# Kernel optimization log

Hardware: AMD Instinct MI355X
Metric: run time of the kernel (lower is better)

## Reference

```python
import jax, jax.numpy as jnp
import numpy as np

NEG = -100000.0  # matches torch masked_fill constant

def setup_inputs() -> dict:
    key = jax.random.key(0)
    k1, k2, k3, k4 = jax.random.split(key, 4)
    B, T, D, H, S = 8, 2048, 1024, 8, 128
    features = jax.random.normal(k1, (B, T, D), dtype=jnp.float32)
    begins = jax.random.randint(k2, (B, S), 0, 2016, dtype=jnp.int64)
    widths = jax.random.randint(k3, (B, S), 1, 33, dtype=jnp.int64)
    ends = jnp.minimum(begins + widths, T)
    key_w = jax.random.normal(k4, (H, D), dtype=jnp.float32) / np.sqrt(D)
    key_b = jnp.zeros((H,), dtype=jnp.float32)
    return {"features": features, "begins": begins, "ends": ends,
            "key_w": key_w, "key_b": key_b}


def reference(features, begins, ends, key_w, key_b):
    # features: [B, T, D]; begins/ends: [B, S]
    B, T, D = features.shape
    H = key_w.shape[0]
    S = begins.shape[1]
    pos = jnp.arange(T)  # [T]
    # span mask [B, S, T]
    mask = (begins[..., None] <= pos) & (pos < ends[..., None])
    # key projection: [B, T, H]
    logits = jnp.einsum('btd,hd->bth', features, key_w) + key_b
    # masked softmax over T per (batch, span, head): [B, S, T, H]
    masked = jnp.where(mask[..., None], logits[:, None, :, :], NEG)
    weights = jax.nn.softmax(masked, axis=-2)
    # values = features reshaped to heads: [B, T, H, D//H]
    values = features.reshape(B, T, H, D // H)
    res = jnp.einsum('bthd,bsth->bshd', values, weights)  # [B, S, H, D//H]
    return res.reshape(B, S, D)
```

## Files before the change

kernel.cpp:

```cpp
#include <hip/hip_runtime.h>

#define B_  8
#define T_  2048
#define D_  1024
#define H_  8
#define S_  128

__global__ __launch_bounds__(1024) void logits_kernel(
    const float* __restrict__ feat,
    const float* __restrict__ kw,
    const float* __restrict__ kb,
    float* __restrict__ logits)
{
    const int wv   = threadIdx.x >> 6;
    const int lane = threadIdx.x & 63;
    const int row  = blockIdx.x * 16 + wv;

    __shared__ __align__(16) float kwl[H_ * D_];

    {
        const float4* src = (const float4*)kw;
        float4*       dst = (float4*)kwl;
        dst[threadIdx.x]        = src[threadIdx.x];
        dst[threadIdx.x + 1024] = src[threadIdx.x + 1024];
    }

    const float* fr = feat + (size_t)row * D_;
    float4 fv0 = *(const float4*)(fr +   0 + lane * 4);
    float4 fv1 = *(const float4*)(fr + 256 + lane * 4);
    float4 fv2 = *(const float4*)(fr + 512 + lane * 4);
    float4 fv3 = *(const float4*)(fr + 768 + lane * 4);

    __syncthreads();

    float acc[H_];
#pragma unroll
    for (int h = 0; h < H_; ++h) {
        const float* kh = &kwl[h * D_ + lane * 4];
        float4 k0 = *(const float4*)(kh +   0);
        float4 k1 = *(const float4*)(kh + 256);
        float4 k2 = *(const float4*)(kh + 512);
        float4 k3 = *(const float4*)(kh + 768);
        acc[h] = fv0.x * k0.x + fv0.y * k0.y + fv0.z * k0.z + fv0.w * k0.w
               + fv1.x * k1.x + fv1.y * k1.y + fv1.z * k1.z + fv1.w * k1.w
               + fv2.x * k2.x + fv2.y * k2.y + fv2.z * k2.z + fv2.w * k2.w
               + fv3.x * k3.x + fv3.y * k3.y + fv3.z * k3.z + fv3.w * k3.w;
    }

#pragma unroll
    for (int s = 0; s < 3; ++s) {
        const int m = 1 << s;
        const bool hi = (lane >> s) & 1;
#pragma unroll
        for (int j = 0; j < (4 >> s); ++j) {
            float mine  = hi ? acc[2 * j + 1] : acc[2 * j];
            float other = hi ? acc[2 * j]     : acc[2 * j + 1];
            acc[j] = mine + __shfl_xor(other, m, 64);
        }
    }
    acc[0] += __shfl_xor(acc[0],  8, 64);
    acc[0] += __shfl_xor(acc[0], 16, 64);
    acc[0] += __shfl_xor(acc[0], 32, 64);

    if (lane < H_)
        logits[(size_t)row * H_ + lane] = acc[0] + kb[lane];
}

__global__ __launch_bounds__(256) void pool_kernel(
    const float* __restrict__ feat,
    const int* __restrict__ begins,
    const int* __restrict__ ends,
    const float* __restrict__ logits,
    float* __restrict__ out)
{
    const int bs   = blockIdx.x;
    const int wv   = threadIdx.x >> 6;
    const int lane = threadIdx.x & 63;
    const int b    = bs >> 7;

    const int begin = begins[bs];
    const int width = ends[bs] - begin;
    const size_t row0 = (size_t)b * T_ + begin;

    float4 lv = *(const float4*)(logits + row0 * H_ + lane * 4);
    const int w8 = width * H_;
    float v0 = (4 * lane + 0 < w8) ? lv.x : -1e30f;
    float v1 = (4 * lane + 1 < w8) ? lv.y : -1e30f;
    float v2 = (4 * lane + 2 < w8) ? lv.z : -1e30f;
    float v3 = (4 * lane + 3 < w8) ? lv.w : -1e30f;

    float m0 = v0, m1 = v1, m2 = v2, m3 = v3;
#pragma unroll
    for (int off = 2; off <= 32; off <<= 1) {
        m0 = fmaxf(m0, __shfl_xor(m0, off, 64));
        m1 = fmaxf(m1, __shfl_xor(m1, off, 64));
        m2 = fmaxf(m2, __shfl_xor(m2, off, 64));
        m3 = fmaxf(m3, __shfl_xor(m3, off, 64));
    }

    float e0 = __expf(v0 - m0);
    float e1 = __expf(v1 - m1);
    float e2 = __expf(v2 - m2);
    float e3 = __expf(v3 - m3);
    float s0 = e0, s1 = e1, s2 = e2, s3 = e3;
#pragma unroll
    for (int off = 2; off <= 32; off <<= 1) {
        s0 += __shfl_xor(s0, off, 64);
        s1 += __shfl_xor(s1, off, 64);
        s2 += __shfl_xor(s2, off, 64);
        s3 += __shfl_xor(s3, off, 64);
    }
    const float w0 = e0 / s0, w1 = e1 / s1, w2 = e2 / s2, w3 = e3 / s3;

    const int p = wv >> 1;
    const float wlo = (wv & 1) ? w2 : w0;
    const float whi = (wv & 1) ? w3 : w1;
    const bool hiHalf = (lane >= 32);

    const int colbase = wv * 256 + lane * 4;
    const float* fbase = feat + row0 * D_ + colbase;

    float4 acc = make_float4(0.f, 0.f, 0.f, 0.f);
    const int nch = (width + 7) >> 3;
    for (int ch = 0; ch < nch; ++ch) {
#pragma unroll
        for (int k = 0; k < 8; ++k) {
            const int i = ch * 8 + k;
            const float t0 = __shfl(wlo, 2 * i + p, 64);
            const float t1 = __shfl(whi, 2 * i + p, 64);
            const float wt = hiHalf ? t1 : t0;
            const float4 fv = *(const float4*)(fbase + (size_t)i * D_);
            acc.x += wt * fv.x;
            acc.y += wt * fv.y;
            acc.z += wt * fv.z;
            acc.w += wt * fv.w;
        }
    }

    *(float4*)(out + (size_t)bs * D_ + colbase) = acc;
}

extern "C" void kernel_launch(void* const* d_in, const int* in_sizes, int n_in,
                              void* d_out, int out_size, void* d_ws, size_t ws_size,
                              hipStream_t stream) {
    const float* feat   = (const float*)d_in[0];
    const int*   begins = (const int*)d_in[1];
    const int*   ends   = (const int*)d_in[2];
    const float* kw     = (const float*)d_in[3];
    const float* kb     = (const float*)d_in[4];
    float*       out    = (float*)d_out;
    float* logits = (float*)d_ws;

    logits_kernel<<<1024, 1024, 0, stream>>>(feat, kw, kb, logits);
    pool_kernel<<<B_ * S_, 256, 0, stream>>>(feat, begins, ends, logits, out);
}
```

Before: 113.1 us.

## Split span pooling across four column-quarter blocks with row-parallel waves

The pool kernel now launches four blocks per span, each covering a quarter of the feature columns. Inside a block the four waves each take a chunk of eight span rows, with their feature loads issued before the softmax. Softmax weights are computed by wave 0 and shared through LDS, and the per-wave partials are summed through LDS. This raises parallelism and memory-level concurrency in the pooling phase, at the cost of recomputing the softmax four times per span plus extra syncs and LDS traffic. Widths are at most 32, so four waves of eight rows cover every span.

```diff
diff --git a/kernel.cpp b/kernel.cpp
--- a/kernel.cpp
+++ b/kernel.cpp
@@ -73,7 +73,9 @@
     const float* __restrict__ logits,
     float* __restrict__ out)
 {
-    const int bs   = blockIdx.x;
+    const int blk  = blockIdx.x;
+    const int bs   = blk >> 2;
+    const int q    = blk & 3;
     const int wv   = threadIdx.x >> 6;
     const int lane = threadIdx.x & 63;
     const int b    = bs >> 7;
@@ -82,62 +84,78 @@
     const int width = ends[bs] - begin;
     const size_t row0 = (size_t)b * T_ + begin;
 
-    float4 lv = *(const float4*)(logits + row0 * H_ + lane * 4);
-    const int w8 = width * H_;
-    float v0 = (4 * lane + 0 < w8) ? lv.x : -1e30f;
-    float v1 = (4 * lane + 1 < w8) ? lv.y : -1e30f;
-    float v2 = (4 * lane + 2 < w8) ? lv.z : -1e30f;
-    float v3 = (4 * lane + 3 < w8) ? lv.w : -1e30f;
+    __shared__ __align__(16) float wslab[256];
+    __shared__ __align__(16) float pslab[4 * 256];
 
-    float m0 = v0, m1 = v1, m2 = v2, m3 = v3;
+    const int colbase = q * 256 + lane * 4;
+    const float* fbase = feat + row0 * D_ + colbase;
+    const bool active = (wv * 8) < width;
+    float4 fv[8];
+    if (active) {
 #pragma unroll
-    for (int off = 2; off <= 32; off <<= 1) {
-        m0 = fmaxf(m0, __shfl_xor(m0, off, 64));
-        m1 = fmaxf(m1, __shfl_xor(m1, off, 64));
-        m2 = fmaxf(m2, __shfl_xor(m2, off, 64));
-        m3 = fmaxf(m3, __shfl_xor(m3, off, 64));
+        for (int k = 0; k < 8; ++k)
+            fv[k] = *(const float4*)(fbase + (size_t)(wv * 8 + k) * D_);
     }
 
-    float e0 = __expf(v0 - m0);
-    float e1 = __expf(v1 - m1);
-    float e2 = __expf(v2 - m2);
-    float e3 = __expf(v3 - m3);
-    float s0 = e0, s1 = e1, s2 = e2, s3 = e3;
+    if (wv == 0) {
+        float4 lv = *(const float4*)(logits + row0 * H_ + lane * 4);
+        const int w8 = width * H_;
+        float v0 = (4 * lane + 0 < w8) ? lv.x : -1e30f;
+        float v1 = (4 * lane + 1 < w8) ? lv.y : -1e30f;
+        float v2 = (4 * lane + 2 < w8) ? lv.z : -1e30f;
+        float v3 = (4 * lane + 3 < w8) ? lv.w : -1e30f;
+
+        float m0 = v0, m1 = v1, m2 = v2, m3 = v3;
 #pragma unroll
-    for (int off = 2; off <= 32; off <<= 1) {
-        s0 += __shfl_xor(s0, off, 64);
-        s1 += __shfl_xor(s1, off, 64);
-        s2 += __shfl_xor(s2, off, 64);
-        s3 += __shfl_xor(s3, off, 64);
+        for (int off = 2; off <= 32; off <<= 1) {
+            m0 = fmaxf(m0, __shfl_xor(m0, off, 64));
+            m1 = fmaxf(m1, __shfl_xor(m1, off, 64));
+            m2 = fmaxf(m2, __shfl_xor(m2, off, 64));
+            m3 = fmaxf(m3, __shfl_xor(m3, off, 64));
+        }
+        float e0 = __expf(v0 - m0);
+        float e1 = __expf(v1 - m1);
+        float e2 = __expf(v2 - m2);
+        float e3 = __expf(v3 - m3);
+        float s0 = e0, s1 = e1, s2 = e2, s3 = e3;
+#pragma unroll
+        for (int off = 2; off <= 32; off <<= 1) {
+            s0 += __shfl_xor(s0, off, 64);
+            s1 += __shfl_xor(s1, off, 64);
+            s2 += __shfl_xor(s2, off, 64);
+            s3 += __shfl_xor(s3, off, 64);
+        }
+        *(float4*)&wslab[lane * 4] =
+            make_float4(e0 / s0, e1 / s1, e2 / s2, e3 / s3);
     }
-    const float w0 = e0 / s0, w1 = e1 / s1, w2 = e2 / s2, w3 = e3 / s3;
-
-    const int p = wv >> 1;
-    const float wlo = (wv & 1) ? w2 : w0;
-    const float whi = (wv & 1) ? w3 : w1;
-    const bool hiHalf = (lane >= 32);
-
-    const int colbase = wv * 256 + lane * 4;
-    const float* fbase = feat + row0 * D_ + colbase;
+    __syncthreads();
 
     float4 acc = make_float4(0.f, 0.f, 0.f, 0.f);
-    const int nch = (width + 7) >> 3;
-    for (int ch = 0; ch < nch; ++ch) {
+    if (active) {
+        const int hoff = 2 * q + (lane >= 32 ? 1 : 0);
 #pragma unroll
         for (int k = 0; k < 8; ++k) {
-            const int i = ch * 8 + k;
-            const float t0 = __shfl(wlo, 2 * i + p, 64);
-            const float t1 = __shfl(whi, 2 * i + p, 64);
-            const float wt = hiHalf ? t1 : t0;
-            const float4 fv = *(const float4*)(fbase + (size_t)i * D_);
-            acc.x += wt * fv.x;
-            acc.y += wt * fv.y;
-            acc.z += wt * fv.z;
-            acc.w += wt * fv.w;
+            const float wt = wslab[(wv * 8 + k) * 8 + hoff];
+            acc.x += wt * fv[k].x;
+            acc.y += wt * fv[k].y;
+            acc.z += wt * fv[k].z;
+            acc.w += wt * fv[k].w;
         }
     }
+    *(float4*)&pslab[wv * 256 + lane * 4] = acc;
+    __syncthreads();
 
-    *(float4*)(out + (size_t)bs * D_ + colbase) = acc;
+    if (wv == 0) {
+        float4 r0 = *(const float4*)&pslab[0 * 256 + lane * 4];
+        float4 r1 = *(const float4*)&pslab[1 * 256 + lane * 4];
+        float4 r2 = *(const float4*)&pslab[2 * 256 + lane * 4];
+        float4 r3 = *(const float4*)&pslab[3 * 256 + lane * 4];
+        float4 o = make_float4(r0.x + r1.x + r2.x + r3.x,
+                               r0.y + r1.y + r2.y + r3.y,
+                               r0.z + r1.z + r2.z + r3.z,
+                               r0.w + r1.w + r2.w + r3.w);
+        *(float4*)(out + (size_t)bs * D_ + colbase) = o;
+    }
 }
 
 extern "C" void kernel_launch(void* const* d_in, const int* in_sizes, int n_in,
@@ -152,5 +170,5 @@
     float* logits = (float*)d_ws;
 
     logits_kernel<<<1024, 1024, 0, stream>>>(feat, kw, kb, logits);
-    pool_kernel<<<B_ * S_, 256, 0, stream>>>(feat, begins, ends, logits, out);
+    pool_kernel<<<B_ * S_ * 4, 256, 0, stream>>>(feat, begins, ends, logits, out);
 }
```

New measurement: 109.4 us. 1.03x faster.
